# Performance work log

Hardware: AMD Instinct MI355X
Metric: run time of the kernel (lower is better)

The kernel has to match this reference:

```python
import jax, jax.numpy as jnp
import numpy as np

STRIDE = 1
PAD = 1
DIL = 1


def setup_inputs() -> dict:
    key = jax.random.key(0)
    k1, k2, k3, k4, k5 = jax.random.split(key, 5)
    B, Cin, D, H, W = 1, 32, 16, 56, 56
    Cout, K = 64, 27  # 3x3x3 kernel
    x = jax.random.normal(k1, (B, Cin, D, H, W), jnp.float32)
    # offset-predicting conv: 3*offset_groups*K output channels (dz,dy,dx per kernel pt)
    # (module inits these to zero; we use small random values to exercise interpolation)
    offset_w = jax.random.normal(k2, (3 * K, Cin, 3, 3, 3), jnp.float32) * 0.02
    offset_b = jax.random.normal(k3, (3 * K,), jnp.float32) * 0.02
    weight = jax.random.normal(k4, (Cout, Cin, 3, 3, 3), jnp.float32) / np.sqrt(Cin * K).astype(np.float32)
    bias = jax.random.normal(k5, (Cout,), jnp.float32) * 0.01
    return {"x": x, "offset_w": offset_w, "offset_b": offset_b, "weight": weight, "bias": bias}


def _trilinear_sample(xc, coords):
    # xc: [C, D, H, W]; coords: [K, P, 3] float (z, y, x) in input voxel space.
    # Zero padding outside bounds (torchvision deform_conv convention).
    C, D, H, W = xc.shape
    xf = xc.reshape(C, D * H * W)
    z, y, x = coords[..., 0], coords[..., 1], coords[..., 2]
    z0, y0, x0 = jnp.floor(z), jnp.floor(y), jnp.floor(x)
    fz, fy, fx = z - z0, y - y0, x - x0
    acc = jnp.zeros((C,) + z.shape, xc.dtype)
    for dz in (0, 1):
        wz = fz if dz else 1.0 - fz
        zi = z0 + dz
        for dy in (0, 1):
            wy = fy if dy else 1.0 - fy
            yi = y0 + dy
            for dx in (0, 1):
                wx = fx if dx else 1.0 - fx
                xi = x0 + dx
                valid = (zi >= 0) & (zi < D) & (yi >= 0) & (yi < H) & (xi >= 0) & (xi < W)
                idx = ((jnp.clip(zi, 0, D - 1) * H + jnp.clip(yi, 0, H - 1)) * W
                       + jnp.clip(xi, 0, W - 1)).astype(jnp.int32)
                w = (wz * wy * wx) * valid.astype(xc.dtype)
                acc = acc + w[None] * xf[:, idx]  # gather -> [C, K, P]
    return acc


def _forward(x, offset_w, offset_b, weight, bias):
    B, Cin, D, H, W = x.shape
    Cout = weight.shape[0]
    kd, kh, kw = weight.shape[2:]
    K = kd * kh * kw
    # dense Conv3d predicting offsets: [B, 3K, Do, Ho, Wo]
    off = jax.lax.conv_general_dilated(
        x, offset_w, (STRIDE,) * 3, [(PAD, PAD)] * 3, rhs_dilation=(DIL,) * 3,
        dimension_numbers=("NCDHW", "OIDHW", "NCDHW")) + offset_b[None, :, None, None, None]
    Do, Ho, Wo = off.shape[2:]
    P = Do * Ho * Wo
    off = off.reshape(B, K, 3, P).transpose(0, 1, 3, 2)  # [B, K, P, 3] (dz,dy,dx)
    # base sampling grid per kernel point
    kz, ky, kx = jnp.meshgrid(jnp.arange(kd), jnp.arange(kh), jnp.arange(kw), indexing="ij")
    kz, ky, kx = kz.reshape(K), ky.reshape(K), kx.reshape(K)
    gz, gy, gx = jnp.meshgrid(jnp.arange(Do) * STRIDE - PAD,
                              jnp.arange(Ho) * STRIDE - PAD,
                              jnp.arange(Wo) * STRIDE - PAD, indexing="ij")
    pz = (kz * DIL)[:, None] + gz.reshape(-1)[None]  # [K, P]
    py = (ky * DIL)[:, None] + gy.reshape(-1)[None]
    px = (kx * DIL)[:, None] + gx.reshape(-1)[None]
    base = jnp.stack([pz, py, px], axis=-1).astype(off.dtype)  # [K, P, 3]
    coords = off + base[None]  # [B, K, P, 3]
    sampled = jax.vmap(_trilinear_sample)(x, coords)  # [B, Cin, K, P]
    out = jnp.einsum("bckp,ock->bop", sampled, weight.reshape(Cout, Cin, K)) + bias[None, :, None]
    return out.reshape(B, Cout, Do, Ho, Wo)


def reference(x, offset_w, offset_b, weight, bias):
    return _forward(x, offset_w, offset_b, weight, bias)
```

## Files before the change

### kernel.cpp

```cpp
#include <hip/hip_runtime.h>
#include <math.h>

#define D_   16
#define H_   56
#define W_   56
#define CIN  32
#define COUT 64
#define KPTS 27
#define NCH  81
#define NP   (D_*H_*W_)
#define CHW  (D_*H_*W_)

typedef float f4 __attribute__((ext_vector_type(4)));

static __device__ __forceinline__ int iclamp(int v, int lo, int hi) {
    return v < lo ? lo : (v > hi ? hi : v);
}

__global__ __launch_bounds__(256) void k_prep(const float* __restrict__ w,
                                              const float* __restrict__ ow,
                                              float* __restrict__ wT,
                                              float* __restrict__ owT) {
    int i = blockIdx.x * 256 + threadIdx.x;
    if (i < COUT * CIN * KPTS) {
        int tap = i % KPTS;
        int c   = (i / KPTS) % CIN;
        int o   = i / (KPTS * CIN);
        wT[(tap * CIN + c) * COUT + o] = w[i];
    }
    if (i < NCH * CIN * KPTS) {
        int tap = i % KPTS;
        int c   = (i / KPTS) % CIN;
        int ch  = i / (KPTS * CIN);
        int d   = ch % 3;
        int k   = ch / 3;
        owT[((tap * CIN + c) * 3 + d) * KPTS + k] = ow[i];
    }
}

__global__ __launch_bounds__(64) void k_xT(const float* __restrict__ x,
                                           float* __restrict__ xT) {
    const int s = blockIdx.x * 64 + threadIdx.x;
    float r[CIN];
#pragma unroll
    for (int c = 0; c < CIN; ++c) r[c] = x[c * CHW + s];
    f4* dst = (f4*)(xT + (size_t)s * CIN);
#pragma unroll
    for (int cc = 0; cc < 8; ++cc) {
        f4 v;
        v.x = r[cc * 4 + 0]; v.y = r[cc * 4 + 1];
        v.z = r[cc * 4 + 2]; v.w = r[cc * 4 + 3];
        dst[cc] = v;
    }
}

__global__ __launch_bounds__(256) void k_init(const float* __restrict__ bias,
                                              float* __restrict__ out) {
    const int i    = blockIdx.x * 256 + threadIdx.x;
    const int idx4 = i * 4;
    const float b  = bias[idx4 / NP];
    f4 v; v.x = b; v.y = b; v.z = b; v.w = b;
    ((f4*)out)[i] = v;
}

__global__ __launch_bounds__(64, 1) void k_offsets(const float* __restrict__ xT,
                                                   const float* __restrict__ owT,
                                                   const float* __restrict__ offb,
                                                   float* __restrict__ coords) {
    const int p  = blockIdx.x * 64 + threadIdx.x;
    const int d  = blockIdx.y;
    const int ox = p % W_;
    const int t  = p / W_;
    const int oy = t % H_;
    const int oz = t / H_;

    float acc[KPTS];
#pragma unroll
    for (int k = 0; k < KPTS; ++k) acc[k] = offb[k * 3 + d];

    for (int tap = 0; tap < KPTS; ++tap) {
        const int kz = tap / 9, ky = (tap / 3) % 3, kx = tap % 3;
        const int zi = oz - 1 + kz, yi = oy - 1 + ky, xi = ox - 1 + kx;
        const bool val = ((unsigned)zi < (unsigned)D_) &&
                         ((unsigned)yi < (unsigned)H_) &&
                         ((unsigned)xi < (unsigned)W_);
        const int zc = iclamp(zi, 0, D_ - 1);
        const int yc = iclamp(yi, 0, H_ - 1);
        const int xc = iclamp(xi, 0, W_ - 1);
        const float m = val ? 1.0f : 0.0f;
        const f4* src = (const f4*)(xT + (size_t)((zc * H_ + yc) * W_ + xc) * CIN);

        f4 xv[8];
#pragma unroll
        for (int cc = 0; cc < 8; ++cc) xv[cc] = src[cc];
#pragma unroll
        for (int cc = 0; cc < 8; ++cc) xv[cc] *= m;

        const float* wp = owT + ((size_t)tap * CIN * 3 + d) * KPTS;
#pragma unroll
        for (int cc = 0; cc < 8; ++cc) {
#pragma unroll
            for (int e = 0; e < 4; ++e) {
                const float xs = (e == 0) ? xv[cc].x : (e == 1) ? xv[cc].y
                                : (e == 2) ? xv[cc].z : xv[cc].w;
                const float* wc = wp + (cc * 4 + e) * (3 * KPTS);
#pragma unroll
                for (int k = 0; k < KPTS; ++k) acc[k] += wc[k] * xs;
            }
        }
    }

    const int bz = oz - 1, by = oy - 1, bx = ox - 1;
#pragma unroll
    for (int k = 0; k < KPTS; ++k) {
        const int kz = k / 9, ky = (k / 3) % 3, kx = k % 3;
        const float base = (d == 0) ? (float)(bz + kz)
                         : (d == 1) ? (float)(by + ky)
                                    : (float)(bx + kx);
        coords[(d * KPTS + k) * NP + p] = acc[k] + base;
    }
}

__global__ __launch_bounds__(64, 1) void k_dconv(const float* __restrict__ xT,
                                                 const float* __restrict__ coords,
                                                 const float* __restrict__ wT,
                                                 float* __restrict__ out) {
    const int p = blockIdx.x * 64 + threadIdx.x;
    const int g = blockIdx.y;

    float acc[COUT];
#pragma unroll
    for (int o = 0; o < COUT; ++o) acc[o] = 0.0f;

    for (int tap = 9 * g; tap < 9 * g + 9; ++tap) {
        const float cz = coords[(0 * KPTS + tap) * NP + p];
        const float cy = coords[(1 * KPTS + tap) * NP + p];
        const float cx = coords[(2 * KPTS + tap) * NP + p];

        const float zf = floorf(cz), yf = floorf(cy), xf = floorf(cx);
        const float fz = cz - zf, fy = cy - yf, fx = cx - xf;
        const int z0 = (int)zf, y0 = (int)yf, x0 = (int)xf;

        float w8[8];
        int   base8[8];
#pragma unroll
        for (int j = 0; j < 8; ++j) {
            const int dz = j >> 2, dy = (j >> 1) & 1, dx = j & 1;
            const int zi = z0 + dz, yi = y0 + dy, xi = x0 + dx;
            const bool v = ((unsigned)zi < (unsigned)D_) &&
                           ((unsigned)yi < (unsigned)H_) &&
                           ((unsigned)xi < (unsigned)W_);
            const float wz = dz ? fz : 1.0f - fz;
            const float wy = dy ? fy : 1.0f - fy;
            const float wx = dx ? fx : 1.0f - fx;
            w8[j] = v ? wz * wy * wx : 0.0f;
            const int zc = iclamp(zi, 0, D_ - 1);
            const int yc = iclamp(yi, 0, H_ - 1);
            const int xc = iclamp(xi, 0, W_ - 1);
            base8[j] = ((zc * H_ + yc) * W_ + xc) * CIN;
        }

        const float* wp = wT + (size_t)tap * CIN * COUT;
        for (int cc = 0; cc < 8; ++cc) {
            f4 s; s.x = 0.f; s.y = 0.f; s.z = 0.f; s.w = 0.f;
#pragma unroll
            for (int j = 0; j < 8; ++j) {
                const f4 v = *(const f4*)(xT + base8[j] + cc * 4);
                s += w8[j] * v;
            }
            const float* wq = wp + cc * 4 * COUT;
#pragma unroll
            for (int e = 0; e < 4; ++e) {
                const float sv = (e == 0) ? s.x : (e == 1) ? s.y
                                : (e == 2) ? s.z : s.w;
#pragma unroll
                for (int o = 0; o < COUT; ++o)
                    acc[o] += wq[e * COUT + o] * sv;
            }
        }
    }

    float* op = out + p;
#pragma unroll
    for (int o = 0; o < COUT; ++o)
        atomicAdd(op + o * NP, acc[o]);
}

extern "C" void kernel_launch(void* const* d_in, const int* in_sizes, int n_in,
                              void* d_out, int out_size, void* d_ws, size_t ws_size,
                              hipStream_t stream) {
    const float* x    = (const float*)d_in[0];
    const float* offw = (const float*)d_in[1];
    const float* offb = (const float*)d_in[2];
    const float* wgt  = (const float*)d_in[3];
    const float* bias = (const float*)d_in[4];
    float* out = (float*)d_out;

    float* ws     = (float*)d_ws;
    float* coords = ws;
    float* wT     = coords + 3 * KPTS * NP;
    float* owT    = wT + KPTS * CIN * COUT;
    float* xT     = owT + KPTS * CIN * 3 * KPTS;

    const int n_tr = NCH * CIN * KPTS;
    hipLaunchKernelGGL(k_prep, dim3((n_tr + 255) / 256), dim3(256), 0, stream,
                       wgt, offw, wT, owT);
    hipLaunchKernelGGL(k_xT, dim3(NP / 64), dim3(64), 0, stream, x, xT);
    hipLaunchKernelGGL(k_init, dim3(COUT * NP / 4 / 256), dim3(256), 0, stream,
                       bias, out);
    hipLaunchKernelGGL(k_offsets, dim3(NP / 64, 3), dim3(64), 0, stream,
                       xT, owT, offb, coords);
    hipLaunchKernelGGL(k_dconv, dim3(NP / 64, 3), dim3(64), 0, stream,
                       xT, coords, wT, out);
}
```

Baseline: 637.2 us.

## Stage per-tap weights in LDS and vectorize accumulators in offset and deform kernels

Both the offset-conv and deformable-conv kernels now copy each tap's weight slice into shared memory, and threads read it back as float4 vectors instead of issuing scalar uniform global loads. Accumulators become f4 registers, and the offset weights are re-laid out with a padded stride of 28 so float4 reads stay aligned. Launch bounds are raised to two blocks per SIMD to improve occupancy. The cost is two barriers per tap and more register pressure, which may cause spills.

```diff
diff --git a/kernel.cpp b/kernel.cpp
--- a/kernel.cpp
+++ b/kernel.cpp
@@ -10,6 +10,7 @@
 #define NCH  81
 #define NP   (D_*H_*W_)
 #define CHW  (D_*H_*W_)
+#define KPAD 28
 
 typedef float f4 __attribute__((ext_vector_type(4)));
 
@@ -33,9 +34,11 @@
         int c   = (i / KPTS) % CIN;
         int ch  = i / (KPTS * CIN);
         int d   = ch % 3;
-        int k   = ch / 3;
-        owT[((tap * CIN + c) * 3 + d) * KPTS + k] = ow[i];
-    }
+        int kpt = ch / 3;
+        owT[(((tap * 3) + d) * CIN + c) * KPAD + kpt] = ow[i];
+    }
+    if (i < KPTS * 3 * CIN)
+        owT[i * KPAD + 27] = 0.0f;
 }
 
 __global__ __launch_bounds__(64) void k_xT(const float* __restrict__ x,
@@ -56,29 +59,45 @@
 
 __global__ __launch_bounds__(256) void k_init(const float* __restrict__ bias,
                                               float* __restrict__ out) {
-    const int i    = blockIdx.x * 256 + threadIdx.x;
-    const int idx4 = i * 4;
-    const float b  = bias[idx4 / NP];
+    const int i   = blockIdx.x * 256 + threadIdx.x;
+    const float b = bias[(i * 4) / NP];
     f4 v; v.x = b; v.y = b; v.z = b; v.w = b;
     ((f4*)out)[i] = v;
 }
 
-__global__ __launch_bounds__(64, 1) void k_offsets(const float* __restrict__ xT,
+__global__ __launch_bounds__(64, 2) void k_offsets(const float* __restrict__ xT,
                                                    const float* __restrict__ owT,
                                                    const float* __restrict__ offb,
                                                    float* __restrict__ coords) {
-    const int p  = blockIdx.x * 64 + threadIdx.x;
-    const int d  = blockIdx.y;
-    const int ox = p % W_;
-    const int t  = p / W_;
-    const int oy = t % H_;
-    const int oz = t / H_;
-
-    float acc[KPTS];
-#pragma unroll
-    for (int k = 0; k < KPTS; ++k) acc[k] = offb[k * 3 + d];
+    __shared__ __align__(16) float lw[CIN * KPAD];
+    const int tid = threadIdx.x;
+    const int p   = blockIdx.x * 64 + tid;
+    const int d   = blockIdx.y;
+    const int ox  = p % W_;
+    const int t   = p / W_;
+    const int oy  = t % H_;
+    const int oz  = t / H_;
+
+    f4 A0, A1, A2, A3, A4, A5, A6;
+#define INIT4(Ai, kb) { f4 v; \
+    v.x = offb[((kb) + 0) * 3 + d]; \
+    v.y = offb[((kb) + 1) * 3 + d]; \
+    v.z = offb[((kb) + 2) * 3 + d]; \
+    v.w = ((kb) + 3 < KPTS) ? offb[((kb) + 3) * 3 + d] : 0.0f; \
+    Ai = v; }
+    INIT4(A0, 0) INIT4(A1, 4) INIT4(A2, 8) INIT4(A3, 12)
+    INIT4(A4, 16) INIT4(A5, 20) INIT4(A6, 24)
+#undef INIT4
 
     for (int tap = 0; tap < KPTS; ++tap) {
+        __syncthreads();
+        {
+            const f4* src4 = (const f4*)(owT + (size_t)((tap * 3 + d) * CIN) * KPAD);
+            f4* lw4 = (f4*)lw;
+            for (int q = tid; q < CIN * KPAD / 4; q += 64) lw4[q] = src4[q];
+        }
+        __syncthreads();
+
         const int kz = tap / 9, ky = (tap / 3) % 3, kx = tap % 3;
         const int zi = oz - 1 + kz, yi = oy - 1 + ky, xi = ox - 1 + kx;
         const bool val = ((unsigned)zi < (unsigned)D_) &&
@@ -90,49 +109,58 @@
         const float m = val ? 1.0f : 0.0f;
         const f4* src = (const f4*)(xT + (size_t)((zc * H_ + yc) * W_ + xc) * CIN);
 
-        f4 xv[8];
-#pragma unroll
-        for (int cc = 0; cc < 8; ++cc) xv[cc] = src[cc];
-#pragma unroll
-        for (int cc = 0; cc < 8; ++cc) xv[cc] *= m;
-
-        const float* wp = owT + ((size_t)tap * CIN * 3 + d) * KPTS;
-#pragma unroll
-        for (int cc = 0; cc < 8; ++cc) {
-#pragma unroll
-            for (int e = 0; e < 4; ++e) {
-                const float xs = (e == 0) ? xv[cc].x : (e == 1) ? xv[cc].y
-                                : (e == 2) ? xv[cc].z : xv[cc].w;
-                const float* wc = wp + (cc * 4 + e) * (3 * KPTS);
-#pragma unroll
-                for (int k = 0; k < KPTS; ++k) acc[k] += wc[k] * xs;
-            }
-        }
-    }
-
-    const int bz = oz - 1, by = oy - 1, bx = ox - 1;
-#pragma unroll
-    for (int k = 0; k < KPTS; ++k) {
-        const int kz = k / 9, ky = (k / 3) % 3, kx = k % 3;
-        const float base = (d == 0) ? (float)(bz + kz)
-                         : (d == 1) ? (float)(by + ky)
-                                    : (float)(bx + kx);
-        coords[(d * KPTS + k) * NP + p] = acc[k] + base;
-    }
-}
-
-__global__ __launch_bounds__(64, 1) void k_dconv(const float* __restrict__ xT,
+        f4 X0 = src[0] * m, X1 = src[1] * m, X2 = src[2] * m, X3 = src[3] * m;
+        f4 X4 = src[4] * m, X5 = src[5] * m, X6 = src[6] * m, X7 = src[7] * m;
+
+        const f4* lw4 = (const f4*)lw;
+#define OF(xs, cfull) { const float s_ = (xs); const f4* wp = lw4 + (cfull) * 7; \
+    A0 += wp[0] * s_; A1 += wp[1] * s_; A2 += wp[2] * s_; A3 += wp[3] * s_; \
+    A4 += wp[4] * s_; A5 += wp[5] * s_; A6 += wp[6] * s_; }
+#define OCC(Xi, cc) { OF(Xi.x, (cc)*4+0) OF(Xi.y, (cc)*4+1) \
+                      OF(Xi.z, (cc)*4+2) OF(Xi.w, (cc)*4+3) }
+        OCC(X0, 0) OCC(X1, 1) OCC(X2, 2) OCC(X3, 3)
+        OCC(X4, 4) OCC(X5, 5) OCC(X6, 6) OCC(X7, 7)
+#undef OCC
+#undef OF
+    }
+
+#define BASEF(kk) ((d == 0) ? (float)(oz - 1 + (kk) / 9) \
+                 : (d == 1) ? (float)(oy - 1 + ((kk) / 3) % 3) \
+                            : (float)(ox - 1 + (kk) % 3))
+#define WOUT(Ai, kb) { \
+    coords[(d * KPTS + (kb) + 0) * NP + p] = Ai.x + BASEF((kb) + 0); \
+    coords[(d * KPTS + (kb) + 1) * NP + p] = Ai.y + BASEF((kb) + 1); \
+    coords[(d * KPTS + (kb) + 2) * NP + p] = Ai.z + BASEF((kb) + 2); \
+    if ((kb) + 3 < KPTS) \
+        coords[(d * KPTS + (kb) + 3) * NP + p] = Ai.w + BASEF((kb) + 3); }
+    WOUT(A0, 0) WOUT(A1, 4) WOUT(A2, 8) WOUT(A3, 12)
+    WOUT(A4, 16) WOUT(A5, 20) WOUT(A6, 24)
+#undef WOUT
+#undef BASEF
+}
+
+__global__ __launch_bounds__(64, 2) void k_dconv(const float* __restrict__ xT,
                                                  const float* __restrict__ coords,
                                                  const float* __restrict__ wT,
                                                  float* __restrict__ out) {
-    const int p = blockIdx.x * 64 + threadIdx.x;
-    const int g = blockIdx.y;
-
-    float acc[COUT];
+    __shared__ __align__(16) float lw[CIN * COUT];
+    const int tid = threadIdx.x;
+    const int p   = blockIdx.x * 64 + tid;
+    const int g   = blockIdx.y;
+
+    f4 A0 = 0, A1 = 0, A2 = 0, A3 = 0, A4 = 0, A5 = 0, A6 = 0, A7 = 0;
+    f4 A8 = 0, A9 = 0, A10 = 0, A11 = 0, A12 = 0, A13 = 0, A14 = 0, A15 = 0;
+
+    for (int tap = 9 * g; tap < 9 * g + 9; ++tap) {
+        __syncthreads();
+        {
+            const f4* s4 = (const f4*)(wT + (size_t)tap * CIN * COUT);
+            f4* l4 = (f4*)lw;
 #pragma unroll
-    for (int o = 0; o < COUT; ++o) acc[o] = 0.0f;
-
-    for (int tap = 9 * g; tap < 9 * g + 9; ++tap) {
+            for (int q0 = 0; q0 < 8; ++q0) l4[q0 * 64 + tid] = s4[q0 * 64 + tid];
+        }
+        __syncthreads();
+
         const float cz = coords[(0 * KPTS + tap) * NP + p];
         const float cy = coords[(1 * KPTS + tap) * NP + p];
         const float cx = coords[(2 * KPTS + tap) * NP + p];
@@ -141,49 +169,56 @@
         const float fz = cz - zf, fy = cy - yf, fx = cx - xf;
         const int z0 = (int)zf, y0 = (int)yf, x0 = (int)xf;
 
-        float w8[8];
-        int   base8[8];
-#pragma unroll
-        for (int j = 0; j < 8; ++j) {
-            const int dz = j >> 2, dy = (j >> 1) & 1, dx = j & 1;
-            const int zi = z0 + dz, yi = y0 + dy, xi = x0 + dx;
-            const bool v = ((unsigned)zi < (unsigned)D_) &&
-                           ((unsigned)yi < (unsigned)H_) &&
-                           ((unsigned)xi < (unsigned)W_);
-            const float wz = dz ? fz : 1.0f - fz;
-            const float wy = dy ? fy : 1.0f - fy;
-            const float wx = dx ? fx : 1.0f - fx;
-            w8[j] = v ? wz * wy * wx : 0.0f;
-            const int zc = iclamp(zi, 0, D_ - 1);
-            const int yc = iclamp(yi, 0, H_ - 1);
-            const int xc = iclamp(xi, 0, W_ - 1);
-            base8[j] = ((zc * H_ + yc) * W_ + xc) * CIN;
-        }
-
-        const float* wp = wT + (size_t)tap * CIN * COUT;
-        for (int cc = 0; cc < 8; ++cc) {
-            f4 s; s.x = 0.f; s.y = 0.f; s.z = 0.f; s.w = 0.f;
-#pragma unroll
-            for (int j = 0; j < 8; ++j) {
-                const f4 v = *(const f4*)(xT + base8[j] + cc * 4);
-                s += w8[j] * v;
-            }
-            const float* wq = wp + cc * 4 * COUT;
-#pragma unroll
-            for (int e = 0; e < 4; ++e) {
-                const float sv = (e == 0) ? s.x : (e == 1) ? s.y
-                                : (e == 2) ? s.z : s.w;
-#pragma unroll
-                for (int o = 0; o < COUT; ++o)
-                    acc[o] += wq[e * COUT + o] * sv;
-            }
-        }
+        float cw0, cw1, cw2, cw3, cw4, cw5, cw6, cw7;
+        int   cb0, cb1, cb2, cb3, cb4, cb5, cb6, cb7;
+#define CORNER(jj, Wj, Bj) { \
+    const int dz_ = (jj) >> 2, dy_ = ((jj) >> 1) & 1, dx_ = (jj) & 1; \
+    const int zi_ = z0 + dz_, yi_ = y0 + dy_, xi_ = x0 + dx_; \
+    const bool v_ = ((unsigned)zi_ < (unsigned)D_) && \
+                    ((unsigned)yi_ < (unsigned)H_) && \
+                    ((unsigned)xi_ < (unsigned)W_); \
+    const float wz_ = dz_ ? fz : 1.0f - fz; \
+    const float wy_ = dy_ ? fy : 1.0f - fy; \
+    const float wx_ = dx_ ? fx : 1.0f - fx; \
+    Wj = v_ ? wz_ * wy_ * wx_ : 0.0f; \
+    Bj = ((iclamp(zi_, 0, D_ - 1) * H_ + iclamp(yi_, 0, H_ - 1)) * W_ \
+          + iclamp(xi_, 0, W_ - 1)) * CIN; }
+        CORNER(0, cw0, cb0) CORNER(1, cw1, cb1) CORNER(2, cw2, cb2)
+        CORNER(3, cw3, cb3) CORNER(4, cw4, cb4) CORNER(5, cw5, cb5)
+        CORNER(6, cw6, cb6) CORNER(7, cw7, cb7)
+#undef CORNER
+
+        const f4* l4 = (const f4*)lw;
+#define LDX(Bj, cc) (*(const f4*)(xT + (Bj) + (cc) * 4))
+#define SFMA(sv, eidx, cc) { const float s_ = (sv); \
+    const f4* wq = l4 + (((cc) * 4 + (eidx)) * 16); \
+    A0  += wq[0]  * s_; A1  += wq[1]  * s_; A2  += wq[2]  * s_; A3  += wq[3]  * s_; \
+    A4  += wq[4]  * s_; A5  += wq[5]  * s_; A6  += wq[6]  * s_; A7  += wq[7]  * s_; \
+    A8  += wq[8]  * s_; A9  += wq[9]  * s_; A10 += wq[10] * s_; A11 += wq[11] * s_; \
+    A12 += wq[12] * s_; A13 += wq[13] * s_; A14 += wq[14] * s_; A15 += wq[15] * s_; }
+#define CCBLK(cc) { \
+    f4 s = cw0 * LDX(cb0, cc); \
+    s += cw1 * LDX(cb1, cc);  s += cw2 * LDX(cb2, cc); \
+    s += cw3 * LDX(cb3, cc);  s += cw4 * LDX(cb4, cc); \
+    s += cw5 * LDX(cb5, cc);  s += cw6 * LDX(cb6, cc); \
+    s += cw7 * LDX(cb7, cc); \
+    SFMA(s.x, 0, cc) SFMA(s.y, 1, cc) SFMA(s.z, 2, cc) SFMA(s.w, 3, cc) }
+        CCBLK(0) CCBLK(1) CCBLK(2) CCBLK(3)
+        CCBLK(4) CCBLK(5) CCBLK(6) CCBLK(7)
+#undef CCBLK
+#undef SFMA
+#undef LDX
     }
 
     float* op = out + p;
-#pragma unroll
-    for (int o = 0; o < COUT; ++o)
-        atomicAdd(op + o * NP, acc[o]);
+#define AOUT(Ai, ob) { \
+    atomicAdd(op + ((ob) + 0) * NP, Ai.x); atomicAdd(op + ((ob) + 1) * NP, Ai.y); \
+    atomicAdd(op + ((ob) + 2) * NP, Ai.z); atomicAdd(op + ((ob) + 3) * NP, Ai.w); }
+    AOUT(A0, 0)  AOUT(A1, 4)  AOUT(A2, 8)   AOUT(A3, 12)
+    AOUT(A4, 16) AOUT(A5, 20) AOUT(A6, 24)  AOUT(A7, 28)
+    AOUT(A8, 32) AOUT(A9, 36) AOUT(A10, 40) AOUT(A11, 44)
+    AOUT(A12, 48) AOUT(A13, 52) AOUT(A14, 56) AOUT(A15, 60)
+#undef AOUT
 }
 
 extern "C" void kernel_launch(void* const* d_in, const int* in_sizes, int n_in,
@@ -200,7 +235,7 @@
     float* coords = ws;
     float* wT     = coords + 3 * KPTS * NP;
     float* owT    = wT + KPTS * CIN * COUT;
-    float* xT     = owT + KPTS * CIN * 3 * KPTS;
+    float* xT     = owT + KPTS * 3 * CIN * KPAD;
 
     const int n_tr = NCH * CIN * KPTS;
     hipLaunchKernelGGL(k_prep, dim3((n_tr + 255) / 256), dim3(256), 0, stream,
```

Result: faster. 544.9 us (-14.5%).
